# Optimization experiments

Hardware: AMD Instinct MI355X
Metric: run time of the kernel (lower is better)

## Reference

```python
import jax, jax.numpy as jnp
import numpy as np


def setup_inputs() -> dict:
    key = jax.random.key(0)
    # [batch, 2 (real/imag), proj_nums, det_nums]
    x = jax.random.normal(key, (16, 2, 1024, 1024), dtype=jnp.float32)
    return {"x": x}


def reference(x) -> jnp.ndarray:
    # Split stacked real/imag channels -> complex frequency-domain sinogram.
    re, im = jnp.split(x, 2, axis=1)          # each [B, 1, P, D]
    c = (re + 1j * im).astype(jnp.complex64)
    # Batched row-wise inverse FFT along detector axis (replaces the
    # per-(batch, row) Python loop of cuFFT calls in the original).
    y = jnp.real(jnp.fft.ifft(jnp.fft.ifftshift(c, axes=-1), axis=-1))
    # Global min-max normalization over the whole tensor.
    y_min = jnp.min(y)
    y_max = jnp.max(y)
    return (y - y_min) / (y_max - y_min)
```

## Files before the change

kernel.cpp:

```cpp
#include <hip/hip_runtime.h>

#define FFT_N   1024
#define NPART   4096

__device__ __forceinline__ int br6(int x) { return (int)(__brev((unsigned)x) >> 26); }

__device__ __forceinline__ unsigned int f2key(float f) {
    unsigned int u = __float_as_uint(f);
    return (u & 0x80000000u) ? ~u : (u | 0x80000000u);
}
__device__ __forceinline__ float key2f(unsigned int k) {
    unsigned int u = (k & 0x80000000u) ? (k & 0x7FFFFFFFu) : ~k;
    return __uint_as_float(u);
}

__global__ void init_mm(unsigned int* mm) {
    mm[0] = 0xFFFFFFFFu;
    mm[1] = 0u;
}

__device__ __constant__ float W16R[10] = {
    1.0f, 0.92387953251f, 0.70710678119f, 0.38268343236f, 0.0f,
    0.0f, -0.70710678119f, 0.0f, 0.0f, -0.92387953251f };
__device__ __constant__ float W16I[10] = {
    0.0f, 0.38268343236f, 0.70710678119f, 0.92387953251f, 1.0f,
    0.0f, 0.70710678119f, 0.0f, 0.0f, -0.38268343236f };

template <bool USE_ATOMIC>
__global__ __launch_bounds__(256) void ifft_rows(const float* __restrict__ x,
                                                 float* __restrict__ out,
                                                 float* __restrict__ partials,
                                                 unsigned int* __restrict__ mm) {
    const int t    = threadIdx.x;
    const int lane = t & 63;
    const int wid  = t >> 6;
    const int row  = blockIdx.x * 4 + wid;
    const int b    = row >> 10;
    const int p    = row & 1023;
    const float* re = x + (((size_t)(b * 2) * 1024) + p) * 1024;
    const float* im = re + (size_t)1024 * 1024;

    const int n1 = br6(lane);

    float xr[16], xi[16];
    #pragma unroll
    for (int r = 0; r < 16; ++r) {
        xr[r] = re[n1 + 64 * r];
        xi[r] = im[n1 + 64 * r];
    }

    float yr[16], yi[16];
    #pragma unroll
    for (int a = 0; a < 4; ++a) {
        float t0r = xr[a] + xr[a + 8],      t0i = xi[a] + xi[a + 8];
        float t1r = xr[a] - xr[a + 8],      t1i = xi[a] - xi[a + 8];
        float t2r = xr[a + 4] + xr[a + 12], t2i = xi[a + 4] + xi[a + 12];
        float t3r = xr[a + 4] - xr[a + 12], t3i = xi[a + 4] - xi[a + 12];
        yr[a]      = t0r + t2r;  yi[a]      = t0i + t2i;
        yr[a + 4]  = t1r - t3i;  yi[a + 4]  = t1i + t3r;
        yr[a + 8]  = t0r - t2r;  yi[a + 8]  = t0i - t2i;
        yr[a + 12] = t1r + t3i;  yi[a + 12] = t1i - t3r;
    }
    float ar_[16], ai_[16];
    #pragma unroll
    for (int c = 0; c < 4; ++c) {
        float zr[4], zi[4];
        #pragma unroll
        for (int a = 0; a < 4; ++a) {
            float wr = W16R[a * c], wi = W16I[a * c];
            float vr = yr[a + 4 * c], vi = yi[a + 4 * c];
            zr[a] = vr * wr - vi * wi;
            zi[a] = vr * wi + vi * wr;
        }
        float u0r = zr[0] + zr[2], u0i = zi[0] + zi[2];
        float u1r = zr[0] - zr[2], u1i = zi[0] - zi[2];
        float u2r = zr[1] + zr[3], u2i = zi[1] + zi[3];
        float u3r = zr[1] - zr[3], u3i = zi[1] - zi[3];
        ar_[c]      = u0r + u2r;  ai_[c]      = u0i + u2i;
        ar_[c + 4]  = u1r - u3i;  ai_[c + 4]  = u1i + u3r;
        ar_[c + 8]  = u0r - u2r;  ai_[c + 8]  = u0i - u2i;
        ar_[c + 12] = u1r + u3i;  ai_[c + 12] = u1i - u3r;
    }

    const float theta = 6.283185307179586f * (float)n1 * (1.0f / 1024.0f);
    #pragma unroll
    for (int k2 = 1; k2 < 16; ++k2) {
        float s, c;
        __sincosf(theta * (float)k2, &s, &c);
        float vr = ar_[k2], vi = ai_[k2];
        ar_[k2] = vr * c - vi * s;
        ai_[k2] = vr * s + vi * c;
    }

    #pragma unroll
    for (int st = 0; st < 6; ++st) {
        const int h = 1 << st;
        const bool odd = (lane & h) != 0;
        float ang = odd ? (3.14159265358979f * (float)(lane & (h - 1)) / (float)h) : 0.0f;
        float ws, wc;
        __sincosf(ang, &ws, &wc);
        const float s = odd ? -1.0f : 1.0f;
        if (st < 5) {
            #pragma unroll
            for (int r = 0; r < 16; ++r) {
                float tr = ar_[r] * wc - ai_[r] * ws;
                float ti = ar_[r] * ws + ai_[r] * wc;
                float pr = __shfl_xor(tr, h);
                float pi = __shfl_xor(ti, h);
                ar_[r] = fmaf(s, tr, pr);
                ai_[r] = fmaf(s, ti, pi);
            }
        } else {
            #pragma unroll
            for (int r = 0; r < 16; ++r) {
                float tr = ar_[r] * wc - ai_[r] * ws;
                float pr = __shfl_xor(tr, h);
                ar_[r] = fmaf(s, tr, pr);
            }
        }
    }

    float vals[16];
    float vmin = INFINITY, vmax = -INFINITY;
    #pragma unroll
    for (int k2 = 0; k2 < 16; ++k2) {
        float v = ar_[k2] * ((k2 & 1) ? -9.765625e-4f : 9.765625e-4f);
        vals[k2] = v;
        vmin = fminf(vmin, v);
        vmax = fmaxf(vmax, v);
    }
    float* orow = out + (size_t)row * FFT_N;
    #pragma unroll
    for (int q = 0; q < 4; ++q) {
        *reinterpret_cast<float4*>(orow + 16 * lane + 4 * q) =
            make_float4(vals[4 * q], vals[4 * q + 1], vals[4 * q + 2], vals[4 * q + 3]);
    }

    #pragma unroll
    for (int off = 32; off >= 1; off >>= 1) {
        vmin = fminf(vmin, __shfl_xor(vmin, off));
        vmax = fmaxf(vmax, __shfl_xor(vmax, off));
    }
    __shared__ float smn[4], smx[4];
    if ((t & 63) == 0) { smn[wid] = vmin; smx[wid] = vmax; }
    __syncthreads();
    if (t == 0) {
        float mn = fminf(fminf(smn[0], smn[1]), fminf(smn[2], smn[3]));
        float mx = fmaxf(fmaxf(smx[0], smx[1]), fmaxf(smx[2], smx[3]));
        if (USE_ATOMIC) {
            atomicMin(&mm[0], f2key(mn));
            atomicMax(&mm[1], f2key(mx));
        } else {
            partials[2 * blockIdx.x]     = mn;
            partials[2 * blockIdx.x + 1] = mx;
        }
    }
}

__global__ __launch_bounds__(256) void reduce_mm(const float* __restrict__ partials,
                                                 float* __restrict__ mm) {
    float mn = INFINITY, mx = -INFINITY;
    for (int i = threadIdx.x; i < NPART; i += 256) {
        float2 v = reinterpret_cast<const float2*>(partials)[i];
        mn = fminf(mn, v.x);
        mx = fmaxf(mx, v.y);
    }
    #pragma unroll
    for (int off = 32; off >= 1; off >>= 1) {
        mn = fminf(mn, __shfl_xor(mn, off));
        mx = fmaxf(mx, __shfl_xor(mx, off));
    }
    __shared__ float smn[4], smx[4];
    const int wid = threadIdx.x >> 6;
    if ((threadIdx.x & 63) == 0) { smn[wid] = mn; smx[wid] = mx; }
    __syncthreads();
    if (threadIdx.x == 0) {
        mm[0] = fminf(fminf(smn[0], smn[1]), fminf(smn[2], smn[3]));
        mm[1] = fmaxf(fmaxf(smx[0], smx[1]), fmaxf(smx[2], smx[3]));
    }
}

template <bool FROM_KEYS>
__global__ __launch_bounds__(256) void normalize_k(float* __restrict__ out,
                                                   const void* __restrict__ mmv,
                                                   int n4) {
    float mn, mx;
    if (FROM_KEYS) {
        const unsigned int* mm = (const unsigned int*)mmv;
        mn = key2f(mm[0]); mx = key2f(mm[1]);
    } else {
        const float* mm = (const float*)mmv;
        mn = mm[0]; mx = mm[1];
    }
    const float inv = 1.0f / (mx - mn);
    float4* o4 = reinterpret_cast<float4*>(out);
    for (int i = blockIdx.x * blockDim.x + threadIdx.x; i < n4;
         i += gridDim.x * blockDim.x) {
        float4 v = o4[i];
        v.x = (v.x - mn) * inv;
        v.y = (v.y - mn) * inv;
        v.z = (v.z - mn) * inv;
        v.w = (v.w - mn) * inv;
        o4[i] = v;
    }
}

extern "C" void kernel_launch(void* const* d_in, const int* in_sizes, int n_in,
                              void* d_out, int out_size, void* d_ws, size_t ws_size,
                              hipStream_t stream) {
    const float* x = (const float*)d_in[0];
    float* out = (float*)d_out;
    const int n4 = out_size / 4;

    if (ws_size >= (size_t)(2 * NPART + 2) * sizeof(float)) {
        float* partials = (float*)d_ws;
        float* mm = partials + 2 * NPART;
        hipLaunchKernelGGL((ifft_rows<false>), dim3(NPART), dim3(256), 0, stream,
                           x, out, partials, nullptr);
        hipLaunchKernelGGL(reduce_mm, dim3(1), dim3(256), 0, stream, partials, mm);
        hipLaunchKernelGGL((normalize_k<false>), dim3(2048), dim3(256), 0, stream,
                           out, (const void*)mm, n4);
    } else {
        unsigned int* mm = (unsigned int*)d_ws;
        hipLaunchKernelGGL(init_mm, dim3(1), dim3(1), 0, stream, mm);
        hipLaunchKernelGGL((ifft_rows<true>), dim3(NPART), dim3(256), 0, stream,
                           x, out, nullptr, mm);
        hipLaunchKernelGGL((normalize_k<true>), dim3(2048), dim3(256), 0, stream,
                           out, (const void*)mm, n4);
    }
}
```

Baseline: 73.38 us.

## Switch IFFT to decimation-in-frequency order with vectorized float4 input loads

Reverses the FFT pipeline so each lane loads 16 contiguous elements with float4 loads instead of bit-reversed strided scalar loads. The cross-lane shuffle stages now run first, followed by twiddles and the in-register radix-16. Output is written as scalar strided stores at bit-reversed positions. The last radix-4 stage computes only real parts and folds the shift sign into one per-lane scale. This trades coalesced vector stores for coalesced vector loads and cuts some arithmetic, but stores become scattered scalar writes.

```diff
diff --git a/kernel.cpp b/kernel.cpp
--- a/kernel.cpp
+++ b/kernel.cpp
@@ -1,7 +1,7 @@
 #include <hip/hip_runtime.h>
 
-#define FFT_N   1024
-#define NPART   4096
+#define FFT_N 1024
+#define NPART 4096
 
 __device__ __forceinline__ int br6(int x) { return (int)(__brev((unsigned)x) >> 26); }
 
@@ -18,13 +18,6 @@
     mm[0] = 0xFFFFFFFFu;
     mm[1] = 0u;
 }
-
-__device__ __constant__ float W16R[10] = {
-    1.0f, 0.92387953251f, 0.70710678119f, 0.38268343236f, 0.0f,
-    0.0f, -0.70710678119f, 0.0f, 0.0f, -0.92387953251f };
-__device__ __constant__ float W16I[10] = {
-    0.0f, 0.38268343236f, 0.70710678119f, 0.92387953251f, 1.0f,
-    0.0f, 0.70710678119f, 0.0f, 0.0f, -0.38268343236f };
 
 template <bool USE_ATOMIC>
 __global__ __launch_bounds__(256) void ifft_rows(const float* __restrict__ x,
@@ -40,100 +33,109 @@
     const float* re = x + (((size_t)(b * 2) * 1024) + p) * 1024;
     const float* im = re + (size_t)1024 * 1024;
 
-    const int n1 = br6(lane);
-
-    float xr[16], xi[16];
-    #pragma unroll
-    for (int r = 0; r < 16; ++r) {
-        xr[r] = re[n1 + 64 * r];
-        xi[r] = im[n1 + 64 * r];
+    float ar[16], ai[16];
+    #pragma unroll
+    for (int q = 0; q < 4; ++q) {
+        float4 v = *reinterpret_cast<const float4*>(re + 16 * lane + 4 * q);
+        ar[4 * q] = v.x; ar[4 * q + 1] = v.y; ar[4 * q + 2] = v.z; ar[4 * q + 3] = v.w;
+    }
+    #pragma unroll
+    for (int q = 0; q < 4; ++q) {
+        float4 w = *reinterpret_cast<const float4*>(im + 16 * lane + 4 * q);
+        ai[4 * q] = w.x; ai[4 * q + 1] = w.y; ai[4 * q + 2] = w.z; ai[4 * q + 3] = w.w;
+    }
+
+    #pragma unroll
+    for (int st = 0; st < 6; ++st) {
+        const int h  = 32 >> st;
+        const bool hi = (lane & h) != 0;
+        const float s = hi ? -1.0f : 1.0f;
+        if (h > 1) {
+            const int j = lane & (h - 1);
+            float ang = hi ? (3.14159265358979323846f / (float)h) * (float)j : 0.0f;
+            float ws, wc;
+            __sincosf(ang, &ws, &wc);
+            #pragma unroll
+            for (int r = 0; r < 16; ++r) {
+                float pr = __shfl_xor(ar[r], h);
+                float pi = __shfl_xor(ai[r], h);
+                float tr = fmaf(s, ar[r], pr);
+                float ti = fmaf(s, ai[r], pi);
+                ar[r] = tr * wc - ti * ws;
+                ai[r] = tr * ws + ti * wc;
+            }
+        } else {
+            #pragma unroll
+            for (int r = 0; r < 16; ++r) {
+                float pr = __shfl_xor(ar[r], 1);
+                float pi = __shfl_xor(ai[r], 1);
+                ar[r] = fmaf(s, ar[r], pr);
+                ai[r] = fmaf(s, ai[r], pi);
+            }
+        }
+    }
+
+    const int k1 = br6(lane);
+    const float theta = 6.283185307179586f * (float)k1 * (1.0f / 1024.0f);
+    #pragma unroll
+    for (int r = 1; r < 16; ++r) {
+        float sn, cs;
+        __sincosf(theta * (float)r, &sn, &cs);
+        float vr = ar[r], vi = ai[r];
+        ar[r] = vr * cs - vi * sn;
+        ai[r] = vr * sn + vi * cs;
     }
 
     float yr[16], yi[16];
     #pragma unroll
     for (int a = 0; a < 4; ++a) {
-        float t0r = xr[a] + xr[a + 8],      t0i = xi[a] + xi[a + 8];
-        float t1r = xr[a] - xr[a + 8],      t1i = xi[a] - xi[a + 8];
-        float t2r = xr[a + 4] + xr[a + 12], t2i = xi[a + 4] + xi[a + 12];
-        float t3r = xr[a + 4] - xr[a + 12], t3i = xi[a + 4] - xi[a + 12];
+        float t0r = ar[a] + ar[a + 8],      t0i = ai[a] + ai[a + 8];
+        float t1r = ar[a] - ar[a + 8],      t1i = ai[a] - ai[a + 8];
+        float t2r = ar[a + 4] + ar[a + 12], t2i = ai[a + 4] + ai[a + 12];
+        float t3r = ar[a + 4] - ar[a + 12], t3i = ai[a + 4] - ai[a + 12];
         yr[a]      = t0r + t2r;  yi[a]      = t0i + t2i;
         yr[a + 4]  = t1r - t3i;  yi[a + 4]  = t1i + t3r;
         yr[a + 8]  = t0r - t2r;  yi[a + 8]  = t0i - t2i;
         yr[a + 12] = t1r + t3i;  yi[a + 12] = t1i - t3r;
     }
-    float ar_[16], ai_[16];
+    constexpr float W16R_[10] = { 1.0f, 0.92387953251f, 0.70710678119f, 0.38268343236f,
+                                  0.0f, 0.0f, -0.70710678119f, 0.0f, 0.0f, -0.92387953251f };
+    constexpr float W16I_[10] = { 0.0f, 0.38268343236f, 0.70710678119f, 0.92387953251f,
+                                  1.0f, 0.0f, 0.70710678119f, 0.0f, 0.0f, -0.38268343236f };
+    float vals[16];
+    const float scale = (lane & 32) ? -9.765625e-4f : 9.765625e-4f;
     #pragma unroll
     for (int c = 0; c < 4; ++c) {
-        float zr[4], zi[4];
-        #pragma unroll
-        for (int a = 0; a < 4; ++a) {
-            float wr = W16R[a * c], wi = W16I[a * c];
-            float vr = yr[a + 4 * c], vi = yi[a + 4 * c];
-            zr[a] = vr * wr - vi * wi;
-            zi[a] = vr * wi + vi * wr;
-        }
-        float u0r = zr[0] + zr[2], u0i = zi[0] + zi[2];
-        float u1r = zr[0] - zr[2], u1i = zi[0] - zi[2];
-        float u2r = zr[1] + zr[3], u2i = zi[1] + zi[3];
-        float u3r = zr[1] - zr[3], u3i = zi[1] - zi[3];
-        ar_[c]      = u0r + u2r;  ai_[c]      = u0i + u2i;
-        ar_[c + 4]  = u1r - u3i;  ai_[c + 4]  = u1i + u3r;
-        ar_[c + 8]  = u0r - u2r;  ai_[c + 8]  = u0i - u2i;
-        ar_[c + 12] = u1r + u3i;  ai_[c + 12] = u1i - u3r;
-    }
-
-    const float theta = 6.283185307179586f * (float)n1 * (1.0f / 1024.0f);
-    #pragma unroll
-    for (int k2 = 1; k2 < 16; ++k2) {
-        float s, c;
-        __sincosf(theta * (float)k2, &s, &c);
-        float vr = ar_[k2], vi = ai_[k2];
-        ar_[k2] = vr * c - vi * s;
-        ai_[k2] = vr * s + vi * c;
-    }
-
-    #pragma unroll
-    for (int st = 0; st < 6; ++st) {
-        const int h = 1 << st;
-        const bool odd = (lane & h) != 0;
-        float ang = odd ? (3.14159265358979f * (float)(lane & (h - 1)) / (float)h) : 0.0f;
-        float ws, wc;
-        __sincosf(ang, &ws, &wc);
-        const float s = odd ? -1.0f : 1.0f;
-        if (st < 5) {
-            #pragma unroll
-            for (int r = 0; r < 16; ++r) {
-                float tr = ar_[r] * wc - ai_[r] * ws;
-                float ti = ar_[r] * ws + ai_[r] * wc;
-                float pr = __shfl_xor(tr, h);
-                float pi = __shfl_xor(ti, h);
-                ar_[r] = fmaf(s, tr, pr);
-                ai_[r] = fmaf(s, ti, pi);
-            }
-        } else {
-            #pragma unroll
-            for (int r = 0; r < 16; ++r) {
-                float tr = ar_[r] * wc - ai_[r] * ws;
-                float pr = __shfl_xor(tr, h);
-                ar_[r] = fmaf(s, tr, pr);
-            }
-        }
-    }
-
-    float vals[16];
+        float zr0 = yr[4 * c];
+        float zr1, zi1, zr2, zr3, zi3;
+        { float wr = W16R_[c],     wi = W16I_[c];
+          float vr = yr[1 + 4 * c], vi = yi[1 + 4 * c];
+          zr1 = vr * wr - vi * wi; zi1 = vr * wi + vi * wr; }
+        { float wr = W16R_[2 * c], wi = W16I_[2 * c];
+          float vr = yr[2 + 4 * c], vi = yi[2 + 4 * c];
+          zr2 = vr * wr - vi * wi; }
+        { float wr = W16R_[3 * c], wi = W16I_[3 * c];
+          float vr = yr[3 + 4 * c], vi = yi[3 + 4 * c];
+          zr3 = vr * wr - vi * wi; zi3 = vr * wi + vi * wr; }
+        float u0r = zr0 + zr2, u1r = zr0 - zr2;
+        float u2r = zr1 + zr3;
+        float u3i = zi1 - zi3;
+        vals[c]      = (u0r + u2r) * scale;
+        vals[c + 4]  = (u1r - u3i) * scale;
+        vals[c + 8]  = (u0r - u2r) * scale;
+        vals[c + 12] = (u1r + u3i) * scale;
+    }
+
     float vmin = INFINITY, vmax = -INFINITY;
     #pragma unroll
     for (int k2 = 0; k2 < 16; ++k2) {
-        float v = ar_[k2] * ((k2 & 1) ? -9.765625e-4f : 9.765625e-4f);
-        vals[k2] = v;
-        vmin = fminf(vmin, v);
-        vmax = fmaxf(vmax, v);
+        vmin = fminf(vmin, vals[k2]);
+        vmax = fmaxf(vmax, vals[k2]);
     }
     float* orow = out + (size_t)row * FFT_N;
     #pragma unroll
-    for (int q = 0; q < 4; ++q) {
-        *reinterpret_cast<float4*>(orow + 16 * lane + 4 * q) =
-            make_float4(vals[4 * q], vals[4 * q + 1], vals[4 * q + 2], vals[4 * q + 3]);
+    for (int k2 = 0; k2 < 16; ++k2) {
+        orow[k1 + (k2 << 6)] = vals[k2];
     }
 
     #pragma unroll
```

Result: no change. 72.69 us (-0.9%).
